# Performance work log

Hardware: AMD Instinct MI355X
Metric: run time of the kernel (lower is better)

Reference implementation:

```python
import jax, jax.numpy as jnp
import numpy as np

BLOCK = 64
# Standard NF4 codebook (bitsandbytes), 16 quantile-based values in [-1, 1].
NF4_CODEBOOK = jnp.array([
    -1.0, -0.6961928009986877, -0.5250730514526367, -0.39491748809814453,
    -0.28444138169288635, -0.18477343022823334, -0.09105003625154495, 0.0,
    0.07958029955625534, 0.16093020141124725, 0.24611230194568634,
    0.33791524171829224, 0.44070982933044434, 0.5626170039176941,
    0.6848514676094055, 1.0], dtype=jnp.float32)


def dequantize_nf4(codes, absmax, shape):
    # codes: int array of 4-bit indices (unpacked), absmax: one scale per BLOCK.
    vals = NF4_CODEBOOK[codes.reshape(-1)]              # [N]
    vals = vals.reshape(-1, BLOCK) * absmax[:, None]    # blockwise rescale
    return vals.reshape(shape)


def setup_inputs() -> dict:
    key = jax.random.key(0)
    k1, k2, k3, k4, k5 = jax.random.split(key, 5)
    B, S, D_IN, D_OUT = 4, 2048, 4096, 4096
    x = jax.random.normal(k1, (B, S, D_IN), dtype=jnp.float32)
    w_codes = jax.random.randint(k2, (D_OUT, D_IN), 0, 16, dtype=jnp.int32)
    w_absmax = jax.random.uniform(k3, (D_OUT * D_IN // BLOCK,), dtype=jnp.float32)
    b_codes = jax.random.randint(k4, (D_OUT,), 0, 16, dtype=jnp.int32)
    b_absmax = jax.random.uniform(k5, (D_OUT // BLOCK,), dtype=jnp.float32)
    return {"x": x, "w_codes": w_codes, "w_absmax": w_absmax,
            "b_codes": b_codes, "b_absmax": b_absmax}


def reference(x, w_codes, w_absmax, b_codes, b_absmax):
    W = dequantize_nf4(w_codes, w_absmax, w_codes.shape)   # [out, in]
    b = dequantize_nf4(b_codes, b_absmax, b_codes.shape)   # [out]
    # F.linear(x, W, b) = x @ W.T + b
    return jnp.einsum('bsd,od->bso', x, W) + b
```

## Files before the change

kernel.cpp:

```cpp
#include <hip/hip_runtime.h>
#include <stdint.h>

typedef __bf16 bf16_t;
typedef __attribute__((ext_vector_type(8))) __bf16 bf16x8;
typedef __attribute__((ext_vector_type(4))) float f32x4;
typedef __attribute__((ext_vector_type(8))) unsigned short ushort8;
typedef __attribute__((ext_vector_type(4))) int int4v;
typedef __attribute__((ext_vector_type(4))) float float4v;

typedef const void __attribute__((address_space(1)))* gptr_t;
typedef void __attribute__((address_space(3)))* lptr_t;

__constant__ float NF4_CB[16] = {
    -1.0f, -0.6961928009986877f, -0.5250730514526367f, -0.39491748809814453f,
    -0.28444138169288635f, -0.18477343022823334f, -0.09105003625154495f, 0.0f,
    0.07958029955625534f, 0.16093020141124725f, 0.24611230194568634f,
    0.33791524171829224f, 0.44070982933044434f, 0.5626170039176941f,
    0.6848514676094055f, 1.0f};

__device__ __forceinline__ unsigned short f32_to_bf16_rne(float f) {
    unsigned int u = __float_as_uint(f);
    u += 0x7FFFu + ((u >> 16) & 1u);
    return (unsigned short)(u >> 16);
}

__global__ void prep_kernel(const int* __restrict__ w_codes,
                            const float* __restrict__ w_absmax,
                            const float* __restrict__ x,
                            const int* __restrict__ b_codes,
                            const float* __restrict__ b_absmax,
                            unsigned short* __restrict__ outW,
                            unsigned short* __restrict__ outA,
                            float* __restrict__ outBias,
                            long w8, long x8, int nbias, long wb, long xb) {
    long blk = blockIdx.x;
    if (blk < wb) {
        long t = blk * blockDim.x + threadIdx.x;
        if (t >= w8) return;
        long base = t * 8;
        float am = w_absmax[t >> 3];
        int4v c0 = *(const int4v*)(w_codes + base);
        int4v c1 = *(const int4v*)(w_codes + base + 4);
        ushort8 v;
        v[0] = f32_to_bf16_rne(NF4_CB[c0[0]] * am);
        v[1] = f32_to_bf16_rne(NF4_CB[c0[1]] * am);
        v[2] = f32_to_bf16_rne(NF4_CB[c0[2]] * am);
        v[3] = f32_to_bf16_rne(NF4_CB[c0[3]] * am);
        v[4] = f32_to_bf16_rne(NF4_CB[c1[0]] * am);
        v[5] = f32_to_bf16_rne(NF4_CB[c1[1]] * am);
        v[6] = f32_to_bf16_rne(NF4_CB[c1[2]] * am);
        v[7] = f32_to_bf16_rne(NF4_CB[c1[3]] * am);
        *(ushort8*)(outW + base) = v;
    } else if (blk < wb + xb) {
        long t = (blk - wb) * blockDim.x + threadIdx.x;
        if (t >= x8) return;
        long base = t * 8;
        float4v f0 = *(const float4v*)(x + base);
        float4v f1 = *(const float4v*)(x + base + 4);
        ushort8 v;
        v[0] = f32_to_bf16_rne(f0[0]);
        v[1] = f32_to_bf16_rne(f0[1]);
        v[2] = f32_to_bf16_rne(f0[2]);
        v[3] = f32_to_bf16_rne(f0[3]);
        v[4] = f32_to_bf16_rne(f1[0]);
        v[5] = f32_to_bf16_rne(f1[1]);
        v[6] = f32_to_bf16_rne(f1[2]);
        v[7] = f32_to_bf16_rne(f1[3]);
        *(ushort8*)(outA + base) = v;
    } else {
        int o = (int)(blk - wb - xb) * blockDim.x + threadIdx.x;
        if (o >= nbias) return;
        outBias[o] = NF4_CB[b_codes[o]] * b_absmax[o >> 6];
    }
}

__global__ void gemm_bias_kernel(const bf16_t* __restrict__ A,
                                 const bf16_t* __restrict__ B,
                                 const float* __restrict__ bias,
                                 float* __restrict__ C,
                                 int M, int N, int K) {
    __shared__ __align__(16) bf16_t sAB[16384];

    const int t = threadIdx.x;
    const int lane = t & 63;
    const int wave = t >> 6;
    const int tileM = blockIdx.y * 128;
    const int tileN = blockIdx.x * 128;

    const int rloc = lane >> 3;
    const int jsw  = (lane & 7) ^ rloc;
    const int chunk0 = wave * 8;
    const int isB = chunk0 >> 4;
    const int ci0 = chunk0 & 15;
    const int r0 = ci0 * 8 + rloc;
    const bf16_t* srcp = (isB ? (B + (size_t)(tileN + r0) * K)
                              : (A + (size_t)(tileM + r0) * K)) + jsw * 8;
    bf16_t* dstp = &sAB[isB * 8192 + ci0 * 512 + lane * 8];
    const size_t srcChunkStride = (size_t)8 * K;

    const int wm = wave >> 1;
    const int wn = wave & 1;
    const int la = lane & 15;
    const int jA = lane >> 4;
    const int jj0 = (jA ^ (lane & 7)) * 8;
    const int aoff = (wm * 64 + la) * 64 + jj0;
    const int boff = 8192 + (wn * 64 + la) * 64 + jj0;

    f32x4 acc[4][4] = {};

    for (int kt = 0; kt < K; kt += 64) {
#pragma unroll
        for (int j8 = 0; j8 < 8; ++j8)
            __builtin_amdgcn_global_load_lds((gptr_t)(srcp + j8 * srcChunkStride),
                                             (lptr_t)(dstp + j8 * 512), 16, 0, 0);
        srcp += 64;
        __syncthreads();

#pragma unroll
        for (int kh = 0; kh < 2; ++kh) {
            const int kx = kh * 32;
            bf16x8 a[4], b[4];
#pragma unroll
            for (int i = 0; i < 4; ++i) a[i] = *(const bf16x8*)&sAB[(aoff + i * 1024) ^ kx];
#pragma unroll
            for (int i = 0; i < 4; ++i) b[i] = *(const bf16x8*)&sAB[(boff + i * 1024) ^ kx];
#pragma unroll
            for (int mi = 0; mi < 4; ++mi)
#pragma unroll
                for (int ni = 0; ni < 4; ++ni)
                    acc[mi][ni] = __builtin_amdgcn_mfma_f32_16x16x32_bf16(
                        a[mi], b[ni], acc[mi][ni], 0, 0, 0);
        }
        __syncthreads();
    }

    const int col0 = tileN + wn * 64 + la;
    const int row0 = tileM + wm * 64 + jA * 4;
    float bv[4];
#pragma unroll
    for (int ni = 0; ni < 4; ++ni) bv[ni] = bias[col0 + ni * 16];
#pragma unroll
    for (int mi = 0; mi < 4; ++mi)
#pragma unroll
        for (int ni = 0; ni < 4; ++ni)
#pragma unroll
            for (int r = 0; r < 4; ++r)
                C[(size_t)(row0 + mi * 16 + r) * N + (col0 + ni * 16)] =
                    acc[mi][ni][r] + bv[ni];
}

extern "C" void kernel_launch(void* const* d_in, const int* in_sizes, int n_in,
                              void* d_out, int out_size, void* d_ws, size_t ws_size,
                              hipStream_t stream) {
    const float* x        = (const float*)d_in[0];
    const int*   w_codes  = (const int*)d_in[1];
    const float* w_absmax = (const float*)d_in[2];
    const int*   b_codes  = (const int*)d_in[3];
    const float* b_absmax = (const float*)d_in[4];
    float* out = (float*)d_out;

    const int  D_OUT = in_sizes[3];
    const long WK    = (long)in_sizes[1];
    const int  D_IN  = (int)(WK / D_OUT);
    const long xN    = (long)in_sizes[0];
    const int  M     = (int)(xN / D_IN);
    const int  N = D_OUT, K = D_IN;

    unsigned short* wsW = (unsigned short*)d_ws;
    unsigned short* wsA = wsW + (size_t)N * K;
    float* wsBias = (float*)(wsA + (size_t)M * K);

    long w8 = WK / 8;
    long x8 = xN / 8;
    long wb = (w8 + 255) / 256;
    long xb = (x8 + 255) / 256;
    long bb = (D_OUT + 255) / 256;
    prep_kernel<<<dim3((unsigned)(wb + xb + bb)), dim3(256), 0, stream>>>(
        w_codes, w_absmax, x, b_codes, b_absmax, wsW, wsA, wsBias,
        w8, x8, D_OUT, wb, xb);

    gemm_bias_kernel<<<dim3(N / 128, M / 128), dim3(256), 0, stream>>>(
        (const bf16_t*)wsA, (const bf16_t*)wsW, wsBias, out, M, N, K);
}
```

Baseline: 522.5 us.

## Use 256x128 GEMM tiles with 8 waves and widen prep to 16 elements

Adds a GEMM variant with 512 threads where each block computes a 256x128 output tile. The B tile is shared across twice as many rows, which cuts redundant global loads of the weight operand. The prep kernel now handles 16 elements per thread and caches the NF4 codebook in shared memory instead of constant memory, to reduce divergent constant lookups. The larger LDS footprint and doubled thread count per block may lower occupancy, and the grid shrinks to half as many blocks.

```diff
diff --git a/kernel.cpp b/kernel.cpp
--- a/kernel.cpp
+++ b/kernel.cpp
@@ -32,55 +32,159 @@
                             unsigned short* __restrict__ outW,
                             unsigned short* __restrict__ outA,
                             float* __restrict__ outBias,
-                            long w8, long x8, int nbias, long wb, long xb) {
+                            long w16, long x16, int nbias, long wb, long xb) {
+    __shared__ float cb[16];
+    if (threadIdx.x < 16) cb[threadIdx.x] = NF4_CB[threadIdx.x];
+    __syncthreads();
+
     long blk = blockIdx.x;
     if (blk < wb) {
         long t = blk * blockDim.x + threadIdx.x;
-        if (t >= w8) return;
-        long base = t * 8;
-        float am = w_absmax[t >> 3];
+        if (t >= w16) return;
+        long base = t * 16;
+        float am = w_absmax[t >> 2];
         int4v c0 = *(const int4v*)(w_codes + base);
         int4v c1 = *(const int4v*)(w_codes + base + 4);
-        ushort8 v;
-        v[0] = f32_to_bf16_rne(NF4_CB[c0[0]] * am);
-        v[1] = f32_to_bf16_rne(NF4_CB[c0[1]] * am);
-        v[2] = f32_to_bf16_rne(NF4_CB[c0[2]] * am);
-        v[3] = f32_to_bf16_rne(NF4_CB[c0[3]] * am);
-        v[4] = f32_to_bf16_rne(NF4_CB[c1[0]] * am);
-        v[5] = f32_to_bf16_rne(NF4_CB[c1[1]] * am);
-        v[6] = f32_to_bf16_rne(NF4_CB[c1[2]] * am);
-        v[7] = f32_to_bf16_rne(NF4_CB[c1[3]] * am);
-        *(ushort8*)(outW + base) = v;
+        int4v c2 = *(const int4v*)(w_codes + base + 8);
+        int4v c3 = *(const int4v*)(w_codes + base + 12);
+        ushort8 v0, v1;
+        v0[0] = f32_to_bf16_rne(cb[c0[0]] * am);
+        v0[1] = f32_to_bf16_rne(cb[c0[1]] * am);
+        v0[2] = f32_to_bf16_rne(cb[c0[2]] * am);
+        v0[3] = f32_to_bf16_rne(cb[c0[3]] * am);
+        v0[4] = f32_to_bf16_rne(cb[c1[0]] * am);
+        v0[5] = f32_to_bf16_rne(cb[c1[1]] * am);
+        v0[6] = f32_to_bf16_rne(cb[c1[2]] * am);
+        v0[7] = f32_to_bf16_rne(cb[c1[3]] * am);
+        v1[0] = f32_to_bf16_rne(cb[c2[0]] * am);
+        v1[1] = f32_to_bf16_rne(cb[c2[1]] * am);
+        v1[2] = f32_to_bf16_rne(cb[c2[2]] * am);
+        v1[3] = f32_to_bf16_rne(cb[c2[3]] * am);
+        v1[4] = f32_to_bf16_rne(cb[c3[0]] * am);
+        v1[5] = f32_to_bf16_rne(cb[c3[1]] * am);
+        v1[6] = f32_to_bf16_rne(cb[c3[2]] * am);
+        v1[7] = f32_to_bf16_rne(cb[c3[3]] * am);
+        *(ushort8*)(outW + base) = v0;
+        *(ushort8*)(outW + base + 8) = v1;
     } else if (blk < wb + xb) {
         long t = (blk - wb) * blockDim.x + threadIdx.x;
-        if (t >= x8) return;
-        long base = t * 8;
+        if (t >= x16) return;
+        long base = t * 16;
         float4v f0 = *(const float4v*)(x + base);
         float4v f1 = *(const float4v*)(x + base + 4);
-        ushort8 v;
-        v[0] = f32_to_bf16_rne(f0[0]);
-        v[1] = f32_to_bf16_rne(f0[1]);
-        v[2] = f32_to_bf16_rne(f0[2]);
-        v[3] = f32_to_bf16_rne(f0[3]);
-        v[4] = f32_to_bf16_rne(f1[0]);
-        v[5] = f32_to_bf16_rne(f1[1]);
-        v[6] = f32_to_bf16_rne(f1[2]);
-        v[7] = f32_to_bf16_rne(f1[3]);
-        *(ushort8*)(outA + base) = v;
+        float4v f2 = *(const float4v*)(x + base + 8);
+        float4v f3 = *(const float4v*)(x + base + 12);
+        ushort8 v0, v1;
+        v0[0] = f32_to_bf16_rne(f0[0]);
+        v0[1] = f32_to_bf16_rne(f0[1]);
+        v0[2] = f32_to_bf16_rne(f0[2]);
+        v0[3] = f32_to_bf16_rne(f0[3]);
+        v0[4] = f32_to_bf16_rne(f1[0]);
+        v0[5] = f32_to_bf16_rne(f1[1]);
+        v0[6] = f32_to_bf16_rne(f1[2]);
+        v0[7] = f32_to_bf16_rne(f1[3]);
+        v1[0] = f32_to_bf16_rne(f2[0]);
+        v1[1] = f32_to_bf16_rne(f2[1]);
+        v1[2] = f32_to_bf16_rne(f2[2]);
+        v1[3] = f32_to_bf16_rne(f2[3]);
+        v1[4] = f32_to_bf16_rne(f3[0]);
+        v1[5] = f32_to_bf16_rne(f3[1]);
+        v1[6] = f32_to_bf16_rne(f3[2]);
+        v1[7] = f32_to_bf16_rne(f3[3]);
+        *(ushort8*)(outA + base) = v0;
+        *(ushort8*)(outA + base + 8) = v1;
     } else {
         int o = (int)(blk - wb - xb) * blockDim.x + threadIdx.x;
         if (o >= nbias) return;
-        outBias[o] = NF4_CB[b_codes[o]] * b_absmax[o >> 6];
-    }
-}
-
-__global__ void gemm_bias_kernel(const bf16_t* __restrict__ A,
-                                 const bf16_t* __restrict__ B,
-                                 const float* __restrict__ bias,
-                                 float* __restrict__ C,
-                                 int M, int N, int K) {
+        outBias[o] = cb[b_codes[o]] * b_absmax[o >> 6];
+    }
+}
+
+__global__ __launch_bounds__(512) void gemm_bias_kernel_256(
+        const bf16_t* __restrict__ A, const bf16_t* __restrict__ B,
+        const float* __restrict__ bias, float* __restrict__ C,
+        int M, int N, int K) {
+    __shared__ __align__(16) bf16_t sAB[24576];
+
+    const int t = threadIdx.x;
+    const int lane = t & 63;
+    const int wave = t >> 6;
+    const int tileM = blockIdx.y * 256;
+    const int tileN = blockIdx.x * 128;
+
+    const int rloc = lane >> 3;
+    const int jsw  = (lane & 7) ^ rloc;
+    const bf16_t* srcp[6];
+    bf16_t* dstp[6];
+#pragma unroll
+    for (int j = 0; j < 6; ++j) {
+        int c = wave * 6 + j;
+        int isB = (c >= 32);
+        int r = (isB ? (c - 32) : c) * 8 + rloc;
+        const bf16_t* base = isB ? (B + (size_t)(tileN + r) * K)
+                                 : (A + (size_t)(tileM + r) * K);
+        srcp[j] = base + jsw * 8;
+        dstp[j] = &sAB[c * 512 + lane * 8];
+    }
+
+    const int wm = wave >> 1;
+    const int wn = wave & 1;
+    const int la = lane & 15;
+    const int jA = lane >> 4;
+    const int jj0 = (jA ^ (lane & 7)) * 8;
+    const int aoff = (wm * 64 + la) * 64 + jj0;
+    const int boff = 16384 + (wn * 64 + la) * 64 + jj0;
+
+    f32x4 acc[4][4] = {};
+
+    for (int kt = 0; kt < K; kt += 64) {
+#pragma unroll
+        for (int j = 0; j < 6; ++j) {
+            __builtin_amdgcn_global_load_lds((gptr_t)(srcp[j]), (lptr_t)(dstp[j]),
+                                             16, 0, 0);
+            srcp[j] += 64;
+        }
+        __syncthreads();
+
+#pragma unroll
+        for (int kh = 0; kh < 2; ++kh) {
+            const int kx = kh * 32;
+            bf16x8 a[4], b[4];
+#pragma unroll
+            for (int i = 0; i < 4; ++i) a[i] = *(const bf16x8*)&sAB[(aoff + i * 1024) ^ kx];
+#pragma unroll
+            for (int i = 0; i < 4; ++i) b[i] = *(const bf16x8*)&sAB[(boff + i * 1024) ^ kx];
+#pragma unroll
+            for (int mi = 0; mi < 4; ++mi)
+#pragma unroll
+                for (int ni = 0; ni < 4; ++ni)
+                    acc[mi][ni] = __builtin_amdgcn_mfma_f32_16x16x32_bf16(
+                        a[mi], b[ni], acc[mi][ni], 0, 0, 0);
+        }
+        __syncthreads();
+    }
+
+    const int col0 = tileN + wn * 64 + la;
+    const int row0 = tileM + wm * 64 + jA * 4;
+    float bv[4];
+#pragma unroll
+    for (int ni = 0; ni < 4; ++ni) bv[ni] = bias[col0 + ni * 16];
+#pragma unroll
+    for (int mi = 0; mi < 4; ++mi)
+#pragma unroll
+        for (int ni = 0; ni < 4; ++ni)
+#pragma unroll
+            for (int r = 0; r < 4; ++r)
+                C[(size_t)(row0 + mi * 16 + r) * N + (col0 + ni * 16)] =
+                    acc[mi][ni][r] + bv[ni];
+}
+
+__global__ void gemm_bias_kernel_128(const bf16_t* __restrict__ A,
+                                     const bf16_t* __restrict__ B,
+                                     const float* __restrict__ bias,
+                                     float* __restrict__ C,
+                                     int M, int N, int K) {
     __shared__ __align__(16) bf16_t sAB[16384];
-
     const int t = threadIdx.x;
     const int lane = t & 63;
     const int wave = t >> 6;
@@ -107,7 +211,6 @@
     const int boff = 8192 + (wn * 64 + la) * 64 + jj0;
 
     f32x4 acc[4][4] = {};
-
     for (int kt = 0; kt < K; kt += 64) {
 #pragma unroll
         for (int j8 = 0; j8 < 8; ++j8)
@@ -115,7 +218,6 @@
                                              (lptr_t)(dstp + j8 * 512), 16, 0, 0);
         srcp += 64;
         __syncthreads();
-
 #pragma unroll
         for (int kh = 0; kh < 2; ++kh) {
             const int kx = kh * 32;
@@ -133,7 +235,6 @@
         }
         __syncthreads();
     }
-
     const int col0 = tileN + wn * 64 + la;
     const int row0 = tileM + wm * 64 + jA * 4;
     float bv[4];
@@ -170,15 +271,20 @@
     unsigned short* wsA = wsW + (size_t)N * K;
     float* wsBias = (float*)(wsA + (size_t)M * K);
 
-    long w8 = WK / 8;
-    long x8 = xN / 8;
-    long wb = (w8 + 255) / 256;
-    long xb = (x8 + 255) / 256;
+    long w16 = WK / 16;
+    long x16 = xN / 16;
+    long wb = (w16 + 255) / 256;
+    long xb = (x16 + 255) / 256;
     long bb = (D_OUT + 255) / 256;
     prep_kernel<<<dim3((unsigned)(wb + xb + bb)), dim3(256), 0, stream>>>(
         w_codes, w_absmax, x, b_codes, b_absmax, wsW, wsA, wsBias,
-        w8, x8, D_OUT, wb, xb);
-
-    gemm_bias_kernel<<<dim3(N / 128, M / 128), dim3(256), 0, stream>>>(
-        (const bf16_t*)wsA, (const bf16_t*)wsW, wsBias, out, M, N, K);
-}
+        w16, x16, D_OUT, wb, xb);
+
+    if (M % 256 == 0) {
+        gemm_bias_kernel_256<<<dim3(N / 128, M / 256), dim3(512), 0, stream>>>(
+            (const bf16_t*)wsA, (const bf16_t*)wsW, wsBias, out, M, N, K);
+    } else {
+        gemm_bias_kernel_128<<<dim3(N / 128, M / 128), dim3(256), 0, stream>>>(
+            (const bf16_t*)wsA, (const bf16_t*)wsW, wsBias, out, M, N, K);
+    }
+}
```

Result: faster. 492.3 us (-5.8%).
